# Optimization experiments

Measured on AMD Instinct MI355X. Metric: run time of the kernel, lower is better.

## Reference

```python
import jax, jax.numpy as jnp
import numpy as np

N = 100000
E = 1000000
D = 32          # numerical_dim
HID = 64        # hidden_dim
OUT = 1         # output_dim
REL = 4 * D     # relation feature dim
EPS = 1e-8


def setup_inputs() -> dict:
    key = jax.random.key(0)
    k_x, k_e, k_w1, k_b1, k_w2, k_b2 = jax.random.split(key, 6)
    x = jax.random.uniform(k_x, (N, D), dtype=jnp.float32)
    edge_index = jax.random.randint(k_e, (2, E), 0, N, dtype=jnp.int64)
    # Linear params (PyTorch convention: W [out, in], y = x @ W.T + b)
    lim1 = 1.0 / np.sqrt(REL)
    W1 = jax.random.uniform(k_w1, (HID, REL), minval=-lim1, maxval=lim1, dtype=jnp.float32)
    b1 = jax.random.uniform(k_b1, (HID,), minval=-lim1, maxval=lim1, dtype=jnp.float32)
    lim2 = 1.0 / np.sqrt(HID)
    W2 = jax.random.uniform(k_w2, (OUT, HID), minval=-lim2, maxval=lim2, dtype=jnp.float32)
    b2 = jax.random.uniform(k_b2, (OUT,), minval=-lim2, maxval=lim2, dtype=jnp.float32)
    return {"x": x, "edge_index": edge_index, "W1": W1, "b1": b1, "W2": W2, "b2": b2}


def _relation_features(x_i, x_j):
    ratio = x_i / (x_j + EPS)
    log_ratio = jnp.log(x_i + EPS) - jnp.log(x_j + EPS)
    abs_diff = jnp.abs(x_i - x_j)
    rel_diff = abs_diff / (jnp.maximum(x_i, x_j) + EPS)
    return jnp.concatenate([ratio, log_ratio, abs_diff, rel_diff], axis=-1)  # [E, 4D]


def reference(x, edge_index, W1, b1, W2, b2):
    src, dst = edge_index[0], edge_index[1]
    x_i = x[src]                      # [E, D] gather source node feats
    x_j = x[dst]                      # [E, D] gather target node feats
    rel = _relation_features(x_i, x_j)  # [E, 4D]
    h = jax.nn.relu(rel @ W1.T + b1)    # [E, HID]
    edge_bias = (h @ W2.T + b2).squeeze(-1)  # [E]
    return edge_bias
```

## Files before the change

kernel.cpp:

```cpp
#include <hip/hip_runtime.h>


#define DD    32
#define HID   64
#define RELF  128
#define EPSF  1e-8f

typedef short  bf16x8 __attribute__((ext_vector_type(8)));
typedef float  f32x4  __attribute__((ext_vector_type(4)));

static __device__ __forceinline__ short bf_rne(float f) {
    unsigned u = __builtin_bit_cast(unsigned, f);
    u += 0x7fffu + ((u >> 16) & 1u);
    return (short)(u >> 16);
}
static __device__ __forceinline__ short bf_tr(float f) {
    return (short)(__builtin_bit_cast(unsigned, f) >> 16);
}
static __device__ __forceinline__ float bf_f(short h) {
    unsigned u = ((unsigned)(unsigned short)h) << 16;
    return __builtin_bit_cast(float, u);
}

__global__ __launch_bounds__(256, 2)
void edge_bias_mfma(const float* __restrict__ x,
                    const int*   __restrict__ ei,
                    const float* __restrict__ W1,
                    const float* __restrict__ b1,
                    const float* __restrict__ W2,
                    const float* __restrict__ b2,
                    float* __restrict__ out,
                    int E)
{
    const int lane = threadIdx.x & 63;
    const int wave = (blockIdx.x * blockDim.x + threadIdx.x) >> 6;
    const int nwv  = (gridDim.x * blockDim.x) >> 6;
    const int c = lane & 15;
    const int q = lane >> 4;

    bf16x8 Bhi[4][4];
    bf16x8 Blo[4];
    #pragma unroll
    for (int nt = 0; nt < 4; ++nt) {
        #pragma unroll
        for (int ks = 0; ks < 4; ++ks) {
            const float* wp = W1 + (nt * 16 + c) * RELF + ks * 32 + q * 8;
            float4 w0 = ((const float4*)wp)[0];
            float4 w1 = ((const float4*)wp)[1];
            float wv[8] = {w0.x, w0.y, w0.z, w0.w, w1.x, w1.y, w1.z, w1.w};
            if (ks == 0) {
                #pragma unroll
                for (int j = 0; j < 8; ++j) {
                    short h = bf_tr(wv[j]);
                    Bhi[nt][0][j] = h;
                    Blo[nt][j]    = bf_rne(wv[j] - bf_f(h));
                }
            } else {
                #pragma unroll
                for (int j = 0; j < 8; ++j)
                    Bhi[nt][ks][j] = bf_rne(wv[j]);
            }
        }
    }
    float b1v[4], w2v[4];
    #pragma unroll
    for (int nt = 0; nt < 4; ++nt) {
        b1v[nt] = b1[nt * 16 + c];
        w2v[nt] = W2[nt * 16 + c];
    }
    const float b2s = b2[0];

    const int ntiles = (E + 15) >> 4;
    for (int t = wave; t < ntiles; t += nwv) {
        const int e0 = t << 4;

        int em = e0 + c; if (em > E - 1) em = E - 1;
        const int src = ei[em];
        const int dst = ei[E + em];
        const float4* pi = (const float4*)(x + (long)src * DD + q * 8);
        const float4* pj = (const float4*)(x + (long)dst * DD + q * 8);
        float4 xi0 = pi[0], xi1 = pi[1];
        float4 xj0 = pj[0], xj1 = pj[1];
        float xiv[8] = {xi0.x, xi0.y, xi0.z, xi0.w, xi1.x, xi1.y, xi1.z, xi1.w};
        float xjv[8] = {xj0.x, xj0.y, xj0.z, xj0.w, xj1.x, xj1.y, xj1.z, xj1.w};

        bf16x8 aRh, aRl, aL, aA, aD;
        #pragma unroll
        for (int j = 0; j < 8; ++j) {
            float xi = xiv[j], xj = xjv[j];
            float ratio = xi * __builtin_amdgcn_rcpf(xj + EPSF);
            float logr  = __logf(xi + EPSF) - __logf(xj + EPSF);
            float ad    = fabsf(xi - xj);
            float rd    = ad * __builtin_amdgcn_rcpf(fmaxf(xi, xj) + EPSF);
            short rh = bf_tr(ratio);
            aRh[j] = rh;
            aRl[j] = bf_rne(ratio - bf_f(rh));
            aL[j]  = bf_rne(logr);
            aA[j]  = bf_rne(ad);
            aD[j]  = bf_rne(rd);
        }

        f32x4 acc[4];
        #pragma unroll
        for (int nt = 0; nt < 4; ++nt) {
            acc[nt][0] = b1v[nt]; acc[nt][1] = b1v[nt];
            acc[nt][2] = b1v[nt]; acc[nt][3] = b1v[nt];
        }
        #pragma unroll
        for (int nt = 0; nt < 4; ++nt) {
            acc[nt] = __builtin_amdgcn_mfma_f32_16x16x32_bf16(aRh, Bhi[nt][0], acc[nt], 0, 0, 0);
            acc[nt] = __builtin_amdgcn_mfma_f32_16x16x32_bf16(aRl, Bhi[nt][0], acc[nt], 0, 0, 0);
            acc[nt] = __builtin_amdgcn_mfma_f32_16x16x32_bf16(aRh, Blo[nt],    acc[nt], 0, 0, 0);
            acc[nt] = __builtin_amdgcn_mfma_f32_16x16x32_bf16(aL,  Bhi[nt][1], acc[nt], 0, 0, 0);
            acc[nt] = __builtin_amdgcn_mfma_f32_16x16x32_bf16(aA,  Bhi[nt][2], acc[nt], 0, 0, 0);
            acc[nt] = __builtin_amdgcn_mfma_f32_16x16x32_bf16(aD,  Bhi[nt][3], acc[nt], 0, 0, 0);
        }

        float p[4];
        #pragma unroll
        for (int r = 0; r < 4; ++r) {
            float pp = 0.f;
            #pragma unroll
            for (int nt = 0; nt < 4; ++nt)
                pp = fmaf(fmaxf(acc[nt][r], 0.f), w2v[nt], pp);
            pp += __shfl_xor(pp, 1);
            pp += __shfl_xor(pp, 2);
            pp += __shfl_xor(pp, 4);
            pp += __shfl_xor(pp, 8);
            p[r] = pp;
        }
        if (c < 4) {
            const int e = e0 + q * 4 + c;
            if (e < E) {
                float v = (c == 0) ? p[0] : (c == 1) ? p[1] : (c == 2) ? p[2] : p[3];
                out[e] = v + b2s;
            }
        }
    }
}

extern "C" void kernel_launch(void* const* d_in, const int* in_sizes, int n_in,
                              void* d_out, int out_size, void* d_ws, size_t ws_size,
                              hipStream_t stream)
{
    const float* x   = (const float*)d_in[0];
    const int*   ei  = (const int*)  d_in[1];
    const float* W1  = (const float*)d_in[2];
    const float* b1  = (const float*)d_in[3];
    const float* W2  = (const float*)d_in[4];
    const float* b2  = (const float*)d_in[5];
    float* out = (float*)d_out;

    const int E = out_size;
    edge_bias_mfma<<<1024, 256, 0, stream>>>(x, ei, W1, b1, W2, b2, out, E);
}
```

Baseline: 154.9 us.

## Precompute per-node bf16 log table and split log-ratio into two MFMAs

Adds a prepass kernel that computes log(x+eps) once per node and stores it as bf16 in the workspace. The edge kernel then gathers these log values for src and dst and feeds them to two MFMAs, one against W1 and one against negated W1, instead of evaluating two logs per element per edge. It also switches several bf16 conversions from round-to-nearest to truncation and packs pairs with v_perm. The cost is one extra launch, an extra gather of 64 bytes per node pair, one more MFMA per tile, and slightly lower precision from truncation.

Result: faster. 151.2 us (-2.4%).

```diff
diff --git a/kernel.cpp b/kernel.cpp
--- a/kernel.cpp
+++ b/kernel.cpp
@@ -9,19 +9,36 @@
 typedef short  bf16x8 __attribute__((ext_vector_type(8)));
 typedef float  f32x4  __attribute__((ext_vector_type(4)));
 
-static __device__ __forceinline__ short bf_rne(float f) {
+union U8 { unsigned u[4]; bf16x8 v; };
+
+static __device__ __forceinline__ unsigned pk_tr(float lo, float hi) {
+    return __builtin_amdgcn_perm(__builtin_bit_cast(unsigned, hi),
+                                 __builtin_bit_cast(unsigned, lo), 0x07060302u);
+}
+static __device__ __forceinline__ unsigned rne_bits(float f) {
     unsigned u = __builtin_bit_cast(unsigned, f);
-    u += 0x7fffu + ((u >> 16) & 1u);
-    return (short)(u >> 16);
-}
-static __device__ __forceinline__ short bf_tr(float f) {
-    return (short)(__builtin_bit_cast(unsigned, f) >> 16);
-}
-static __device__ __forceinline__ float bf_f(short h) {
-    unsigned u = ((unsigned)(unsigned short)h) << 16;
-    return __builtin_bit_cast(float, u);
-}
-
+    return u + 0x7fffu + ((u >> 16) & 1u);
+}
+static __device__ __forceinline__ unsigned pk_rne(float lo, float hi) {
+    return __builtin_amdgcn_perm(rne_bits(hi), rne_bits(lo), 0x07060302u);
+}
+static __device__ __forceinline__ float hi_f32(float f) {
+    return __builtin_bit_cast(float, __builtin_bit_cast(unsigned, f) & 0xffff0000u);
+}
+
+__global__ __launch_bounds__(256)
+void prep_logx(const float* __restrict__ x, unsigned* __restrict__ lx, int nq)
+{
+    int i = blockIdx.x * blockDim.x + threadIdx.x;
+    if (i >= nq) return;
+    float4 v = ((const float4*)x)[i];
+    uint2 o;
+    o.x = pk_rne(__logf(v.x + EPSF), __logf(v.y + EPSF));
+    o.y = pk_rne(__logf(v.z + EPSF), __logf(v.w + EPSF));
+    ((uint2*)lx)[i] = o;
+}
+
+template <int PRE>
 __global__ __launch_bounds__(256, 2)
 void edge_bias_mfma(const float* __restrict__ x,
                     const int*   __restrict__ ei,
@@ -29,6 +46,7 @@
                     const float* __restrict__ b1,
                     const float* __restrict__ W2,
                     const float* __restrict__ b2,
+                    const short* __restrict__ lx,
                     float* __restrict__ out,
                     int E)
 {
@@ -38,29 +56,33 @@
     const int c = lane & 15;
     const int q = lane >> 4;
 
-    bf16x8 Bhi[4][4];
-    bf16x8 Blo[4];
+    bf16x8 W0h[4], W0l[4], WL[4], WLn[4], WA[4], WDm[4];
     #pragma unroll
     for (int nt = 0; nt < 4; ++nt) {
-        #pragma unroll
-        for (int ks = 0; ks < 4; ++ks) {
-            const float* wp = W1 + (nt * 16 + c) * RELF + ks * 32 + q * 8;
-            float4 w0 = ((const float4*)wp)[0];
-            float4 w1 = ((const float4*)wp)[1];
-            float wv[8] = {w0.x, w0.y, w0.z, w0.w, w1.x, w1.y, w1.z, w1.w};
-            if (ks == 0) {
-                #pragma unroll
-                for (int j = 0; j < 8; ++j) {
-                    short h = bf_tr(wv[j]);
-                    Bhi[nt][0][j] = h;
-                    Blo[nt][j]    = bf_rne(wv[j] - bf_f(h));
-                }
-            } else {
-                #pragma unroll
-                for (int j = 0; j < 8; ++j)
-                    Bhi[nt][ks][j] = bf_rne(wv[j]);
-            }
-        }
+        const float* wr = W1 + (nt * 16 + c) * RELF + q * 8;
+        U8 h, l, t;
+        #pragma unroll
+        for (int p = 0; p < 4; ++p) {
+            float w0 = wr[2 * p], w1 = wr[2 * p + 1];
+            h.u[p] = pk_tr(w0, w1);
+            l.u[p] = pk_rne(w0 - hi_f32(w0), w1 - hi_f32(w1));
+        }
+        W0h[nt] = h.v; W0l[nt] = l.v;
+        #pragma unroll
+        for (int p = 0; p < 4; ++p)
+            t.u[p] = pk_rne(wr[32 + 2 * p], wr[32 + 2 * p + 1]);
+        WL[nt] = t.v;
+        #pragma unroll
+        for (int p = 0; p < 4; ++p) t.u[p] ^= 0x80008000u;
+        WLn[nt] = t.v;
+        #pragma unroll
+        for (int p = 0; p < 4; ++p)
+            t.u[p] = pk_rne(wr[64 + 2 * p], wr[64 + 2 * p + 1]);
+        WA[nt] = t.v;
+        #pragma unroll
+        for (int p = 0; p < 4; ++p)
+            t.u[p] = pk_rne(wr[96 + 2 * p], wr[96 + 2 * p + 1]);
+        WDm[nt] = t.v;
     }
     float b1v[4], w2v[4];
     #pragma unroll
@@ -73,31 +95,45 @@
     const int ntiles = (E + 15) >> 4;
     for (int t = wave; t < ntiles; t += nwv) {
         const int e0 = t << 4;
-
         int em = e0 + c; if (em > E - 1) em = E - 1;
         const int src = ei[em];
         const int dst = ei[E + em];
-        const float4* pi = (const float4*)(x + (long)src * DD + q * 8);
-        const float4* pj = (const float4*)(x + (long)dst * DD + q * 8);
-        float4 xi0 = pi[0], xi1 = pi[1];
-        float4 xj0 = pj[0], xj1 = pj[1];
+
+        const float* pxi = x + (long)src * DD + q * 8;
+        const float* pxj = x + (long)dst * DD + q * 8;
+        float4 xi0 = ((const float4*)pxi)[0], xi1 = ((const float4*)pxi)[1];
+        float4 xj0 = ((const float4*)pxj)[0], xj1 = ((const float4*)pxj)[1];
         float xiv[8] = {xi0.x, xi0.y, xi0.z, xi0.w, xi1.x, xi1.y, xi1.z, xi1.w};
         float xjv[8] = {xj0.x, xj0.y, xj0.z, xj0.w, xj1.x, xj1.y, xj1.z, xj1.w};
 
-        bf16x8 aRh, aRl, aL, aA, aD;
-        #pragma unroll
-        for (int j = 0; j < 8; ++j) {
-            float xi = xiv[j], xj = xjv[j];
-            float ratio = xi * __builtin_amdgcn_rcpf(xj + EPSF);
-            float logr  = __logf(xi + EPSF) - __logf(xj + EPSF);
-            float ad    = fabsf(xi - xj);
-            float rd    = ad * __builtin_amdgcn_rcpf(fmaxf(xi, xj) + EPSF);
-            short rh = bf_tr(ratio);
-            aRh[j] = rh;
-            aRl[j] = bf_rne(ratio - bf_f(rh));
-            aL[j]  = bf_rne(logr);
-            aA[j]  = bf_rne(ad);
-            aD[j]  = bf_rne(rd);
+        bf16x8 aLi, aLj;
+        if constexpr (PRE) {
+            aLi = *(const bf16x8*)(lx + (long)src * DD + q * 8);
+            aLj = *(const bf16x8*)(lx + (long)dst * DD + q * 8);
+        } else {
+            U8 ti, tj;
+            #pragma unroll
+            for (int p = 0; p < 4; ++p) {
+                ti.u[p] = pk_rne(__logf(xiv[2*p] + EPSF), __logf(xiv[2*p+1] + EPSF));
+                tj.u[p] = pk_rne(__logf(xjv[2*p] + EPSF), __logf(xjv[2*p+1] + EPSF));
+            }
+            aLi = ti.v; aLj = tj.v;
+        }
+
+        U8 R, Rl, Aa, Dd;
+        #pragma unroll
+        for (int p = 0; p < 4; ++p) {
+            float a0 = xiv[2*p], a1 = xiv[2*p+1];
+            float c0 = xjv[2*p], c1 = xjv[2*p+1];
+            float r0 = a0 * __builtin_amdgcn_rcpf(c0 + EPSF);
+            float r1 = a1 * __builtin_amdgcn_rcpf(c1 + EPSF);
+            float d0 = fabsf(a0 - c0), d1 = fabsf(a1 - c1);
+            float g0 = d0 * __builtin_amdgcn_rcpf(fmaxf(a0, c0) + EPSF);
+            float g1 = d1 * __builtin_amdgcn_rcpf(fmaxf(a1, c1) + EPSF);
+            R.u[p]  = pk_tr(r0, r1);
+            Rl.u[p] = pk_tr(r0 - hi_f32(r0), r1 - hi_f32(r1));
+            Aa.u[p] = pk_tr(d0, d1);
+            Dd.u[p] = pk_tr(g0, g1);
         }
 
         f32x4 acc[4];
@@ -108,12 +144,13 @@
         }
         #pragma unroll
         for (int nt = 0; nt < 4; ++nt) {
-            acc[nt] = __builtin_amdgcn_mfma_f32_16x16x32_bf16(aRh, Bhi[nt][0], acc[nt], 0, 0, 0);
-            acc[nt] = __builtin_amdgcn_mfma_f32_16x16x32_bf16(aRl, Bhi[nt][0], acc[nt], 0, 0, 0);
-            acc[nt] = __builtin_amdgcn_mfma_f32_16x16x32_bf16(aRh, Blo[nt],    acc[nt], 0, 0, 0);
-            acc[nt] = __builtin_amdgcn_mfma_f32_16x16x32_bf16(aL,  Bhi[nt][1], acc[nt], 0, 0, 0);
-            acc[nt] = __builtin_amdgcn_mfma_f32_16x16x32_bf16(aA,  Bhi[nt][2], acc[nt], 0, 0, 0);
-            acc[nt] = __builtin_amdgcn_mfma_f32_16x16x32_bf16(aD,  Bhi[nt][3], acc[nt], 0, 0, 0);
+            acc[nt] = __builtin_amdgcn_mfma_f32_16x16x32_bf16(R.v,  W0h[nt], acc[nt], 0, 0, 0);
+            acc[nt] = __builtin_amdgcn_mfma_f32_16x16x32_bf16(Rl.v, W0h[nt], acc[nt], 0, 0, 0);
+            acc[nt] = __builtin_amdgcn_mfma_f32_16x16x32_bf16(R.v,  W0l[nt], acc[nt], 0, 0, 0);
+            acc[nt] = __builtin_amdgcn_mfma_f32_16x16x32_bf16(aLi,  WL[nt],  acc[nt], 0, 0, 0);
+            acc[nt] = __builtin_amdgcn_mfma_f32_16x16x32_bf16(aLj,  WLn[nt], acc[nt], 0, 0, 0);
+            acc[nt] = __builtin_amdgcn_mfma_f32_16x16x32_bf16(Aa.v, WA[nt],  acc[nt], 0, 0, 0);
+            acc[nt] = __builtin_amdgcn_mfma_f32_16x16x32_bf16(Dd.v, WDm[nt], acc[nt], 0, 0, 0);
         }
 
         float p[4];
@@ -151,6 +188,16 @@
     const float* b2  = (const float*)d_in[5];
     float* out = (float*)d_out;
 
-    const int E = out_size;
-    edge_bias_mfma<<<1024, 256, 0, stream>>>(x, ei, W1, b1, W2, b2, out, E);
-}
+    const int E  = out_size;
+    const int Nd = in_sizes[0];
+    short* lx = (short*)d_ws;
+
+    const bool pre = ws_size >= (size_t)Nd * sizeof(short) && (Nd % 4) == 0;
+    if (pre) {
+        const int nq = Nd / 4;
+        prep_logx<<<(nq + 255) / 256, 256, 0, stream>>>(x, (unsigned*)lx, nq);
+        edge_bias_mfma<1><<<1024, 256, 0, stream>>>(x, ei, W1, b1, W2, b2, lx, out, E);
+    } else {
+        edge_bias_mfma<0><<<1024, 256, 0, stream>>>(x, ei, W1, b1, W2, b2, lx, out, E);
+    }
+}
```
